# Kernel optimization log

Hardware: AMD Instinct MI355X
Metric: run time of the kernel (lower is better)

Reference implementation:

```python
import jax, jax.numpy as jnp
import numpy as np

B = 2
H = 112
W = 112
C = 256
NHEAD = 8
SW = 7          # strip width
WIN = 2 * SW    # 14, window size of attn3
L = H * W
HID = 4 * C     # mlp hidden


def _rel_pos_index(wh, ww):
    coords = np.stack(np.meshgrid(np.arange(wh), np.arange(ww), indexing='ij'))  # (2, wh, ww)
    cf = coords.reshape(2, -1)
    rel = (cf[:, :, None] - cf[:, None, :]).transpose(1, 2, 0)  # (N, N, 2)
    rel[:, :, 0] += wh - 1
    rel[:, :, 1] += ww - 1
    rel[:, :, 0] *= 2 * ww - 1
    return rel.sum(-1)  # (N, N) int


def setup_inputs() -> dict:
    key = jax.random.key(0)
    ks = jax.random.split(key, 16)
    s = 0.02
    d = {}
    d['x'] = jax.random.normal(ks[0], (B, L, C), jnp.float32)
    d['g1'] = jnp.ones((C,), jnp.float32); d['b1'] = jnp.zeros((C,), jnp.float32)
    d['g2'] = jnp.ones((C,), jnp.float32); d['b2'] = jnp.zeros((C,), jnp.float32)
    for i, p in enumerate(['a1', 'a2', 'a3']):
        d[p + '_wqkv'] = jax.random.normal(ks[1 + i], (C, 3 * C), jnp.float32) * s
        d[p + '_wproj'] = jax.random.normal(ks[4 + i], (C, C), jnp.float32) * s
        d[p + '_bproj'] = jnp.zeros((C,), jnp.float32)
    d['a3_rpb'] = jax.random.normal(ks[7], ((2 * WIN - 1) * (2 * WIN - 1), NHEAD), jnp.float32) * s
    d['w_fc1'] = jax.random.normal(ks[8], (C, HID), jnp.float32) * s
    d['b_fc1'] = jnp.zeros((HID,), jnp.float32)
    d['w_fc2'] = jax.random.normal(ks[9], (HID, C), jnp.float32) * s
    d['b_fc2'] = jnp.zeros((C,), jnp.float32)
    return d


def _ln(x, g, b):
    m = x.mean(-1, keepdims=True)
    v = jnp.mean((x - m) ** 2, axis=-1, keepdims=True)
    return (x - m) * jax.lax.rsqrt(v + 1e-5) * g + b


def _mha(xw, wqkv, wproj, bproj, bias=None):
    # xw: (Bw, N, C) -> vanilla MHA within each window
    Bw, N, Cc = xw.shape
    hd = Cc // NHEAD
    qkv = (xw @ wqkv).reshape(Bw, N, 3, NHEAD, hd).transpose(2, 0, 3, 1, 4)
    q, k, v = qkv[0], qkv[1], qkv[2]
    attn = jnp.einsum('bhnd,bhmd->bhnm', q, k) * (hd ** -0.5)
    if bias is not None:
        attn = attn + bias
    attn = jax.nn.softmax(attn, axis=-1)
    out = jnp.einsum('bhnm,bhmd->bhnd', attn, v).transpose(0, 2, 1, 3).reshape(Bw, N, Cc)
    return out @ wproj + bproj


def _forward(x, g1, b1, g2, b2,
             a1_wqkv, a1_wproj, a1_bproj,
             a2_wqkv, a2_wproj, a2_bproj,
             a3_wqkv, a3_wproj, a3_bproj, a3_rpb,
             w_fc1, b_fc1, w_fc2, b_fc2):
    shortcut = x
    xn = _ln(x, g1, b1)
    xg = xn.reshape(B, H, W, C)

    # attn1: horizontal strips, window (SW, W) -> seq SW*W
    xh = xg.reshape(B * (H // SW), SW * W, C)
    x1 = _mha(xh, a1_wqkv, a1_wproj, a1_bproj).reshape(B, L, C)

    # attn2: vertical strips, window (H, SW) -> seq H*SW
    xv = xg.reshape(B, H, W // SW, SW, C).transpose(0, 2, 1, 3, 4).reshape(B * (W // SW), H * SW, C)
    x2 = _mha(xv, a2_wqkv, a2_wproj, a2_bproj)
    x2 = x2.reshape(B, W // SW, H, SW, C).transpose(0, 2, 1, 3, 4).reshape(B, L, C)

    # attn3: 14x14 windows with relative position bias
    xw = xg.reshape(B, H // WIN, WIN, W // WIN, WIN, C).transpose(0, 1, 3, 2, 4, 5).reshape(-1, WIN * WIN, C)
    rpi = jnp.asarray(_rel_pos_index(WIN, WIN).reshape(-1))
    bias = a3_rpb[rpi].reshape(WIN * WIN, WIN * WIN, NHEAD).transpose(2, 0, 1)[None]  # (1,h,N,N)
    x3 = _mha(xw, a3_wqkv, a3_wproj, a3_bproj, bias=bias)
    x3 = x3.reshape(B, H // WIN, W // WIN, WIN, WIN, C).transpose(0, 1, 3, 2, 4, 5).reshape(B, L, C)

    # attention-based aggregation of the three branches (per token)
    kx = jnp.stack([x1, x2, x3], axis=2)                      # (B, L, 3, C)
    scores = jnp.einsum('blc,blkc->blk', xn, kx) * (C ** -0.5)
    wts = jax.nn.softmax(scores, axis=-1)
    f = jnp.einsum('blk,blkc->blc', wts, kx)

    x = shortcut + f
    h = jax.nn.gelu(_ln(x, g2, b2) @ w_fc1 + b_fc1, approximate=False) @ w_fc2 + b_fc2
    return x + h


def reference(x, g1, b1, g2, b2,
              a1_wqkv, a1_wproj, a1_bproj,
              a2_wqkv, a2_wproj, a2_bproj,
              a3_wqkv, a3_wproj, a3_bproj, a3_rpb,
              w_fc1, b_fc1, w_fc2, b_fc2):
    return _forward(x, g1, b1, g2, b2,
                    a1_wqkv, a1_wproj, a1_bproj,
                    a2_wqkv, a2_wproj, a2_bproj,
                    a3_wqkv, a3_wproj, a3_bproj, a3_rpb,
                    w_fc1, b_fc1, w_fc2, b_fc2)
```

## Files before the change

kernel.cpp:

```cpp
#include <hip/hip_runtime.h>
#include <hip/hip_bf16.h>

#define M_TOK   25088
#define C_DIM   256
#define NH      8
#define HID_DIM 1024
#define PSTR    40
#define ASTR    40
#define LOG2E   1.4426950408889634f
#define MC_ELT  ((size_t)M_TOK * C_DIM)

typedef __attribute__((ext_vector_type(8))) short short8;
typedef __attribute__((ext_vector_type(4))) short short4v;
typedef __attribute__((ext_vector_type(4))) float f32x4;
typedef __attribute__((ext_vector_type(4))) unsigned u32x4;

__device__ __forceinline__ short f2bf(float f) {
    return __builtin_bit_cast(short, __float2bfloat16(f));
}
__device__ __forceinline__ float bf2f(short s) {
    return __bfloat162float(__builtin_bit_cast(__hip_bfloat16, s));
}

__device__ __forceinline__ int xcd_swz(int orig, int nwg) {
    int q = nwg >> 3, r = nwg & 7;
    int xcd = orig & 7, sub = orig >> 3;
    return (xcd < r ? xcd * (q + 1) : r * (q + 1) + (xcd - r) * q) + sub;
}

__device__ __forceinline__ int map_t(int branch, int w, int n) {
    if (branch == 0) {
        return w * 784 + n;
    } else if (branch == 1) {
        int b = w >> 4, wc = w & 15;
        int h2 = n / 7, s = n - h2 * 7;
        return b * 12544 + h2 * 112 + wc * 7 + s;
    } else {
        int b = w >> 6, wi = w & 63;
        int wh = wi >> 3, ww = wi & 7;
        int i = n / 14, j = n - i * 14;
        return b * 12544 + (wh * 14 + i) * 112 + ww * 14 + j;
    }
}

__device__ __forceinline__ int win2tok(int br, int m) {
    if (br == 0) return m;
    if (br == 1) { int w = m / 784, n = m - w * 784; return map_t(1, w, n); }
    int w = m / 196, n = m - w * 196; return map_t(2, w, n);
}

template<int BR>
__device__ __forceinline__ void tok2win(int t, int& w, int& n) {
    if constexpr (BR == 0) {
        w = t / 784; n = t - w * 784;
    } else if constexpr (BR == 1) {
        int b = t / 12544, r = t - b * 12544;
        int h2 = r / 112, cc = r - h2 * 112;
        int wc = cc / 7, s = cc - wc * 7;
        w = b * 16 + wc; n = h2 * 7 + s;
    } else {
        int b = t / 12544, r = t - b * 12544;
        int ii = r / 112, jj = r - ii * 112;
        int wh = ii / 14, i = ii - wh * 14;
        int ww = jj / 14, j = jj - ww * 14;
        w = b * 64 + wh * 8 + ww; n = i * 14 + j;
    }
}
__device__ __forceinline__ void tok2win_rt(int br, int t, int& w, int& n) {
    if (br == 0) tok2win<0>(t, w, n);
    else if (br == 1) tok2win<1>(t, w, n);
    else tok2win<2>(t, w, n);
}

__global__ void detect_kernel(const unsigned* __restrict__ g1, int* flag) {
    if (threadIdx.x == 0) *flag = (g1[0] == 0x3F800000u) ? 1 : 0;
}

struct PrepArgs {
    const void* src[9];
    short* dst[9];
    int n[9];
};
__global__ void prep_kernel(PrepArgs a, const int* __restrict__ flag) {
    int i = blockIdx.x * 256 + threadIdx.x;
    int fp32 = *flag;
    #pragma unroll
    for (int s = 0; s < 9; ++s) {
        if (i < a.n[s]) {
            a.dst[s][i] = fp32 ? f2bf(((const float*)a.src[s])[i])
                               : ((const short*)a.src[s])[i];
            return;
        }
        i -= a.n[s];
    }
}

__global__ void biasmat_kernel(const void* __restrict__ rpbr,
                               short* __restrict__ bmat,
                               const int* __restrict__ flag) {
    int idx = blockIdx.x * 256 + threadIdx.x;
    if (idx >= 8 * 196 * 196) return;
    int h = idx / 38416, rest = idx - h * 38416;
    int n1 = rest / 196, n2 = rest - n1 * 196;
    int i1 = n1 / 14, j1 = n1 - i1 * 14;
    int i2 = n2 / 14, j2 = n2 - i2 * 14;
    int src = ((i1 - i2 + 13) * 27 + (j1 - j2 + 13)) * 8 + h;
    float v = *flag ? ((const float*)rpbr)[src] : bf2f(((const short*)rpbr)[src]);
    bmat[idx] = f2bf(v * LOG2E);
}

__global__ __launch_bounds__(256) void ln_kernel(
    const void* __restrict__ x, const short* __restrict__ g,
    const short* __restrict__ b, short* __restrict__ out,
    const int* __restrict__ flag)
{
    int t = blockIdx.x * 4 + (threadIdx.x >> 6);
    int lane = threadIdx.x & 63;
    size_t base = (size_t)t * C_DIM + lane * 4;
    float v[4];
    if (*flag) {
        f32x4 hv = *(const f32x4*)((const float*)x + base);
        #pragma unroll
        for (int j = 0; j < 4; ++j) v[j] = hv[j];
    } else {
        short4v hv = *(const short4v*)((const short*)x + base);
        #pragma unroll
        for (int j = 0; j < 4; ++j) v[j] = bf2f(hv[j]);
    }
    float s = v[0] + v[1] + v[2] + v[3];
    float ss = v[0]*v[0] + v[1]*v[1] + v[2]*v[2] + v[3]*v[3];
    for (int off = 32; off; off >>= 1) {
        s  += __shfl_xor(s, off);
        ss += __shfl_xor(ss, off);
    }
    float mean = s * (1.f / 256.f);
    float var  = fmaxf(ss * (1.f / 256.f) - mean * mean, 0.f);
    float rstd = rsqrtf(var + 1e-5f);
    short4v hg = *(const short4v*)(g + lane * 4);
    short4v hb = *(const short4v*)(b + lane * 4);
    short4v o;
    #pragma unroll
    for (int j = 0; j < 4; ++j)
        o[j] = f2bf((v[j] - mean) * rstd * bf2f(hg[j]) + bf2f(hb[j]));
    *(short4v*)(out + base) = o;
}

struct TJobs {
    const void* src[8];
    short* dst[8];
    int R[8], C[8], sc[8], tx[8];
    int pre[9];
    float smul;
};
__global__ void transpose_all_kernel(TJobs jb, const int* __restrict__ flag)
{
    __shared__ short tile[32][33];
    int b = blockIdx.x;
    int j = 0;
    while (b >= jb.pre[j + 1]) ++j;
    int local = b - jb.pre[j];
    int tX = jb.tx[j];
    int c0 = (local % tX) * 32, r0 = (local / tX) * 32;
    const void* src = jb.src[j];
    short* dst = jb.dst[j];
    int R = jb.R[j], Cc = jb.C[j], scaleCols = jb.sc[j];
    int tx_ = threadIdx.x, ty_ = threadIdx.y;
    int fp32 = *flag;
    #pragma unroll
    for (int i = 0; i < 32; i += 8) {
        int r = r0 + ty_ + i, c = c0 + tx_;
        if (r < R && c < Cc) {
            size_t idx = (size_t)r * Cc + c;
            float v = fp32 ? ((const float*)src)[idx] : bf2f(((const short*)src)[idx]);
            if (c < scaleCols) v *= jb.smul;
            tile[ty_ + i][tx_] = f2bf(v);
        }
    }
    __syncthreads();
    #pragma unroll
    for (int i = 0; i < 32; i += 8) {
        int r = c0 + ty_ + i, c = r0 + tx_;
        if (r < Cc && c < R) dst[(size_t)r * R + c] = tile[tx_][ty_ + i];
    }
}

__device__ __forceinline__ float fast_gelu(float v) {
    float v2 = v * v;
    float a = v * (2.30221856f + 0.102948668f * v2);
    float e2 = __builtin_amdgcn_exp2f(-a);
    return v * __builtin_amdgcn_rcpf(1.f + e2);
}

template<int QKV>
__global__ __launch_bounds__(512, 4) void gemm256_kernel(
    const short* __restrict__ A, const short* __restrict__ Bt,
    short* __restrict__ Out, int Nn, int Kk,
    const short* __restrict__ bias, int act, short* __restrict__ qkvb)
{
    __shared__ alignas(16) short As[2][256 * ASTR];
    __shared__ alignas(16) short Bs[2][128 * ASTR];
    int tid = threadIdx.x;
    int lane = tid & 63, wid = tid >> 6;
    int wrow = (wid >> 1) * 64, wcol = (wid & 1) * 64;
    int r16 = lane & 15, q4 = lane >> 4;

    int gX = gridDim.x;
    int nwg = gX * gridDim.y;
    int wgid = xcd_swz(blockIdx.y * gX + blockIdx.x, nwg);
    int bx = wgid % gX, by = wgid / gX;
    int mb = by * 256, nb = bx * 128;

    int arow = tid >> 1, ash = (tid & 1) * 16;
    int brow = tid >> 2, bsh = (tid & 3) * 8;
    const short* Ag = A  + (size_t)(mb + arow) * Kk + ash;
    const short* Bg = Bt + (size_t)(nb + brow) * Kk + bsh;
    short* Al = &As[0][arow * ASTR + ash];
    short* Bl = &Bs[0][brow * ASTR + bsh];

    f32x4 acc[4][4];
    #pragma unroll
    for (int i = 0; i < 4; ++i)
        #pragma unroll
        for (int j = 0; j < 4; ++j)
            acc[i][j] = (f32x4){0.f, 0.f, 0.f, 0.f};

    {
        short8 a0 = *(const short8*)(Ag);
        short8 a1 = *(const short8*)(Ag + 8);
        short8 b0 = *(const short8*)(Bg);
        *(short8*)(Al)     = a0;
        *(short8*)(Al + 8) = a1;
        *(short8*)(Bl)     = b0;
    }
    __syncthreads();

    int nk = Kk >> 5;
    for (int ki = 0; ki < nk; ++ki) {
        int cur = ki & 1;
        bool pref = (ki + 1 < nk);
        short8 na0, na1, nb0;
        if (pref) {
            int k0 = (ki + 1) << 5;
            na0 = *(const short8*)(Ag + k0);
            na1 = *(const short8*)(Ag + k0 + 8);
            nb0 = *(const short8*)(Bg + k0);
        }
        const short* Ar = &As[cur][0];
        const short* Br = &Bs[cur][0];
        short8 af[4], bf[4];
        #pragma unroll
        for (int mi = 0; mi < 4; ++mi)
            af[mi] = *(const short8*)(Ar + (wrow + mi * 16 + r16) * ASTR + q4 * 8);
        #pragma unroll
        for (int ni = 0; ni < 4; ++ni)
            bf[ni] = *(const short8*)(Br + (wcol + ni * 16 + r16) * ASTR + q4 * 8);
        __builtin_amdgcn_s_setprio(1);
        #pragma unroll
        for (int mi = 0; mi < 4; ++mi)
            #pragma unroll
            for (int ni = 0; ni < 4; ++ni)
                acc[mi][ni] = __builtin_amdgcn_mfma_f32_16x16x32_bf16(af[mi], bf[ni], acc[mi][ni], 0, 0, 0);
        __builtin_amdgcn_s_setprio(0);
        if (pref) {
            *(short8*)(Al + (cur ^ 1) * (256 * ASTR))     = na0;
            *(short8*)(Al + (cur ^ 1) * (256 * ASTR) + 8) = na1;
            *(short8*)(Bl + (cur ^ 1) * (128 * ASTR))     = nb0;
        }
        __syncthreads();
    }

    if constexpr (QKV == 0) {
        #pragma unroll
        for (int mi = 0; mi < 4; ++mi) {
            #pragma unroll
            for (int ni = 0; ni < 4; ++ni) {
                int n = nb + wcol + ni * 16 + r16;
                float bval = bias ? bf2f(bias[n]) : 0.f;
                #pragma unroll
                for (int r = 0; r < 4; ++r) {
                    int m = mb + wrow + mi * 16 + q4 * 4 + r;
                    float v = acc[mi][ni][r] + bval;
                    if (act == 1) v = fast_gelu(v);
                    Out[(size_t)m * Nn + n] = f2bf(v);
                }
            }
        }
    } else {
        int brq = nb / 768;
        int rem = nb - brq * 768;
        int sel = rem >> 8;
        int colb = rem & 255;
        int Nw = (brq == 2) ? 196 : 784;
        short* dst = qkvb + ((size_t)brq * 3 + sel) * MC_ELT + colb;
        #pragma unroll
        for (int mi = 0; mi < 4; ++mi) {
            #pragma unroll
            for (int r = 0; r < 4; ++r) {
                int m = mb + wrow + mi * 16 + q4 * 4 + r;
                int w, nwin;
                tok2win_rt(brq, m, w, nwin);
                size_t row = (size_t)(w * Nw + nwin) * 256;
                #pragma unroll
                for (int ni = 0; ni < 4; ++ni)
                    dst[row + wcol + ni * 16 + r16] = f2bf(acc[mi][ni][r]);
            }
        }
    }
}

__global__ __launch_bounds__(256) void gemm128_kernel(
    const short* __restrict__ A, const short* __restrict__ Bt,
    void* __restrict__ Out, int Nn, int Kk,
    const short* __restrict__ bias, const short* __restrict__ res,
    const int* __restrict__ oflag)
{
    __shared__ alignas(16) short As[2][128 * ASTR];
    __shared__ alignas(16) short Bs[2][128 * ASTR];
    int tid = threadIdx.x;
    int lane = tid & 63, wid = tid >> 6;
    int wrow = (wid >> 1) * 64, wcol = (wid & 1) * 64;
    int r16 = lane & 15, q4 = lane >> 4;

    int gX = gridDim.x;
    int nwg = gX * gridDim.y;
    int wgid = xcd_swz(blockIdx.y * gX + blockIdx.x, nwg);
    int bx = wgid % gX, by = wgid / gX;
    int mb = by * 128, nb = bx * 128;

    int srow = tid >> 1, sh = (tid & 1) * 16;
    const short* Ag = A  + (size_t)(mb + srow) * Kk + sh;
    const short* Bg = Bt + (size_t)(nb + srow) * Kk + sh;
    short* Al = &As[0][srow * ASTR + sh];
    short* Bl = &Bs[0][srow * ASTR + sh];

    f32x4 acc[4][4];
    #pragma unroll
    for (int i = 0; i < 4; ++i)
        #pragma unroll
        for (int j = 0; j < 4; ++j)
            acc[i][j] = (f32x4){0.f, 0.f, 0.f, 0.f};

    {
        short8 a0 = *(const short8*)(Ag);
        short8 a1 = *(const short8*)(Ag + 8);
        short8 b0 = *(const short8*)(Bg);
        short8 b1 = *(const short8*)(Bg + 8);
        *(short8*)(Al)     = a0;
        *(short8*)(Al + 8) = a1;
        *(short8*)(Bl)     = b0;
        *(short8*)(Bl + 8) = b1;
    }
    __syncthreads();

    int nk = Kk >> 5;
    for (int ki = 0; ki < nk; ++ki) {
        int cur = ki & 1;
        bool pref = (ki + 1 < nk);
        short8 na0, na1, nb0, nb1;
        if (pref) {
            int k0 = (ki + 1) << 5;
            na0 = *(const short8*)(Ag + k0);
            na1 = *(const short8*)(Ag + k0 + 8);
            nb0 = *(const short8*)(Bg + k0);
            nb1 = *(const short8*)(Bg + k0 + 8);
        }
        const short* Ar = &As[cur][0];
        const short* Br = &Bs[cur][0];
        short8 af[4], bf[4];
        #pragma unroll
        for (int mi = 0; mi < 4; ++mi)
            af[mi] = *(const short8*)(Ar + (wrow + mi * 16 + r16) * ASTR + q4 * 8);
        #pragma unroll
        for (int ni = 0; ni < 4; ++ni)
            bf[ni] = *(const short8*)(Br + (wcol + ni * 16 + r16) * ASTR + q4 * 8);
        __builtin_amdgcn_s_setprio(1);
        #pragma unroll
        for (int mi = 0; mi < 4; ++mi)
            #pragma unroll
            for (int ni = 0; ni < 4; ++ni)
                acc[mi][ni] = __builtin_amdgcn_mfma_f32_16x16x32_bf16(af[mi], bf[ni], acc[mi][ni], 0, 0, 0);
        __builtin_amdgcn_s_setprio(0);
        if (pref) {
            int off2 = (cur ^ 1) * (128 * ASTR);
            *(short8*)(Al + off2)     = na0;
            *(short8*)(Al + off2 + 8) = na1;
            *(short8*)(Bl + off2)     = nb0;
            *(short8*)(Bl + off2 + 8) = nb1;
        }
        __syncthreads();
    }

    int ofp32 = oflag ? *oflag : 0;
    #pragma unroll
    for (int mi = 0; mi < 4; ++mi) {
        #pragma unroll
        for (int ni = 0; ni < 4; ++ni) {
            int n = nb + wcol + ni * 16 + r16;
            float bval = bias ? bf2f(bias[n]) : 0.f;
            #pragma unroll
            for (int r = 0; r < 4; ++r) {
                int m = mb + wrow + mi * 16 + q4 * 4 + r;
                float v = acc[mi][ni][r] + bval;
                if (res) v += bf2f(res[(size_t)m * Nn + n]);
                size_t oi = (size_t)m * Nn + n;
                if (ofp32) ((float*)Out)[oi] = v;
                else       ((short*)Out)[oi] = f2bf(v);
            }
        }
    }
}

__global__ __launch_bounds__(256) void gemm_proj_kernel(
    const short* __restrict__ awb, const short* __restrict__ wprojT,
    const short* __restrict__ bproj3, short* __restrict__ pbb)
{
    __shared__ alignas(16) short As[2][128 * ASTR];
    __shared__ alignas(16) short Bs[2][128 * ASTR];
    int tid = threadIdx.x;
    int lane = tid & 63, wid = tid >> 6;
    int wrow = (wid >> 1) * 64, wcol = (wid & 1) * 64;
    int r16 = lane & 15, q4 = lane >> 4;
    int br = blockIdx.z;

    const short* A  = awb + (size_t)br * MC_ELT;
    const short* Bt = wprojT + (size_t)br * 256 * 256;
    const short* bias = bproj3 + br * 256;
    short* Out = pbb + (size_t)br * MC_ELT;

    int gX = gridDim.x;
    int nwg = gX * gridDim.y;
    int wgid = xcd_swz(blockIdx.y * gX + blockIdx.x, nwg);
    int bx = wgid % gX, by = wgid / gX;
    int mb = by * 128, nb = bx * 128;

    int srow = tid >> 1, sh = (tid & 1) * 16;
    const short* Ag = A  + (size_t)(mb + srow) * 256 + sh;
    const short* Bg = Bt + (size_t)(nb + srow) * 256 + sh;
    short* Al = &As[0][srow * ASTR + sh];
    short* Bl = &Bs[0][srow * ASTR + sh];

    f32x4 acc[4][4];
    #pragma unroll
    for (int i = 0; i < 4; ++i)
        #pragma unroll
        for (int j = 0; j < 4; ++j)
            acc[i][j] = (f32x4){0.f, 0.f, 0.f, 0.f};

    {
        short8 a0 = *(const short8*)(Ag);
        short8 a1 = *(const short8*)(Ag + 8);
        short8 b0 = *(const short8*)(Bg);
        short8 b1 = *(const short8*)(Bg + 8);
        *(short8*)(Al)     = a0;
        *(short8*)(Al + 8) = a1;
        *(short8*)(Bl)     = b0;
        *(short8*)(Bl + 8) = b1;
    }
    __syncthreads();

    #pragma unroll
    for (int ki = 0; ki < 8; ++ki) {
        int cur = ki & 1;
        bool pref = (ki + 1 < 8);
        short8 na0, na1, nb0, nb1;
        if (pref) {
            int k0 = (ki + 1) << 5;
            na0 = *(const short8*)(Ag + k0);
            na1 = *(const short8*)(Ag + k0 + 8);
            nb0 = *(const short8*)(Bg + k0);
            nb1 = *(const short8*)(Bg + k0 + 8);
        }
        const short* Ar = &As[cur][0];
        const short* Br = &Bs[cur][0];
        short8 af[4], bf[4];
        #pragma unroll
        for (int mi = 0; mi < 4; ++mi)
            af[mi] = *(const short8*)(Ar + (wrow + mi * 16 + r16) * ASTR + q4 * 8);
        #pragma unroll
        for (int ni = 0; ni < 4; ++ni)
            bf[ni] = *(const short8*)(Br + (wcol + ni * 16 + r16) * ASTR + q4 * 8);
        __builtin_amdgcn_s_setprio(1);
        #pragma unroll
        for (int mi = 0; mi < 4; ++mi)
            #pragma unroll
            for (int ni = 0; ni < 4; ++ni)
                acc[mi][ni] = __builtin_amdgcn_mfma_f32_16x16x32_bf16(af[mi], bf[ni], acc[mi][ni], 0, 0, 0);
        __builtin_amdgcn_s_setprio(0);
        if (pref) {
            int off2 = (cur ^ 1) * (128 * ASTR);
            *(short8*)(Al + off2)     = na0;
            *(short8*)(Al + off2 + 8) = na1;
            *(short8*)(Bl + off2)     = nb0;
            *(short8*)(Bl + off2 + 8) = nb1;
        }
        __syncthreads();
    }

    #pragma unroll
    for (int mi = 0; mi < 4; ++mi) {
        #pragma unroll
        for (int r = 0; r < 4; ++r) {
            int m = mb + wrow + mi * 16 + q4 * 4 + r;
            int t = win2tok(br, m);
            size_t row = (size_t)t * 256;
            #pragma unroll
            for (int ni = 0; ni < 4; ++ni) {
                int n = nb + wcol + ni * 16 + r16;
                Out[row + n] = f2bf(acc[mi][ni][r] + bf2f(bias[n]));
            }
        }
    }
}

__global__ __launch_bounds__(256) void attn_kernel(
    const short* __restrict__ qkvb, const short* __restrict__ bmat,
    short* __restrict__ awb)
{
    __shared__ alignas(16) short kbuf[2][64 * PSTR];
    __shared__ alignas(16) short vbuf[2][2048];

    int tid = threadIdx.x;
    int lane = tid & 63, wid = tid >> 6;
    int bid = xcd_swz(blockIdx.x, gridDim.x);
    int br, N, QC;
    const short* bmp = nullptr;
    if (bid < 1792)      { br = 0; N = 784; QC = 7; }
    else if (bid < 3584) { br = 1; N = 784; QC = 7; bid -= 1792; }
    else                 { br = 2; N = 196; QC = 2; bid -= 3584; bmp = bmat; }
    const short* qw = qkvb + (size_t)br * 3 * MC_ELT;
    const short* kw = qw + MC_ELT;
    const short* vw = qw + 2 * MC_ELT;
    short* aw = awb + (size_t)br * MC_ELT;

    int t2 = bid / QC;
    int qc = bid - t2 * QC;
    int h = t2 & 7;
    int w = t2 >> 3;
    int qt = qc * 4 + wid;
    int r16 = lane & 15, q4 = lane >> 4;
    int wbase = w * N;
    int QT = (N + 31) >> 5;
    bool active = (qt < QT);

    const short* kws = kw + (size_t)wbase * 256 + h * 32;
    const short* vws = vw + (size_t)wbase * 256 + h * 32;

    int s_row = tid >> 2, s_seg = tid & 3;
    int s_k = s_row & 31;
    int Lr = (s_row >> 5) * 32 + ((s_k & 15) >> 2) * 8 + (s_k >> 4) * 4 + (s_k & 3);
    short* kdst = &kbuf[0][s_row * PSTR + s_seg * 8];
    short* vdst = &vbuf[0][(s_seg >> 1) * 1024 + Lr * 16 + (s_seg & 1) * 8];
    const short* ksrc = kws + s_seg * 8;
    const short* vsrc = vws + s_seg * 8;

    int qr0 = qt * 32 + r16;      if (qr0 >= N) qr0 = N - 1;
    int qr1 = qt * 32 + 16 + r16; if (qr1 >= N) qr1 = N - 1;
    short8 aq0 = *(const short8*)(qw + (size_t)(wbase + qr0) * 256 + h * 32 + q4 * 8);
    short8 aq1 = *(const short8*)(qw + (size_t)(wbase + qr1) * 256 + h * 32 + q4 * 8);

    f32x4 o00 = {0.f,0.f,0.f,0.f}, o01 = o00, o10 = o00, o11 = o00;
    float psA = 0.f, psB = 0.f;
    const short* bra = nullptr; const short* brb = nullptr;
    if (bmp) {
        const short* bh = bmp + (size_t)h * 38416;
        int n1a = qt * 32 + r16;      if (n1a >= N) n1a = N - 1;
        int n1b = qt * 32 + 16 + r16; if (n1b >= N) n1b = N - 1;
        bra = bh + n1a * 196;
        brb = bh + n1b * 196;
    }
    f32x4 zero = {0.f,0.f,0.f,0.f};
    unsigned vb0 = (unsigned)(unsigned long long)(&vbuf[0][0]) + q4 * 256 + r16 * 2;

    int nch = (N + 63) >> 6;
    {
        *(short8*)kdst = *(const short8*)(ksrc + (size_t)s_row * 256);
        *(short8*)vdst = *(const short8*)(vsrc + (size_t)s_row * 256);
    }
    __syncthreads();

    for (int cb = 0; cb < nch; ++cb) {
        int cur = cb & 1;
        bool pref = (cb + 1 < nch);
        short8 kreg, vreg;
        if (pref) {
            int r = (cb + 1) * 64 + s_row; if (r >= N) r = N - 1;
            kreg = *(const short8*)(ksrc + (size_t)r * 256);
            vreg = *(const short8*)(vsrc + (size_t)r * 256);
        }
        if (active) {
            int kb0 = cb * 64;
            int kb1 = kb0 + 32;
            bool act1 = (kb1 < N);
            const short* kbc = &kbuf[cur][0];
            short8 bk00 = *(const short8*)(kbc + r16 * PSTR + q4 * 8);
            short8 bk01 = *(const short8*)(kbc + (16 + r16) * PSTR + q4 * 8);
            short8 bk10 = *(const short8*)(kbc + (32 + r16) * PSTR + q4 * 8);
            short8 bk11 = *(const short8*)(kbc + (48 + r16) * PSTR + q4 * 8);
            unsigned va = vb0 + cur * 4096;
            short4v t00, t01, t02, t03, t10, t11, t12, t13;
            asm volatile("ds_read_b64_tr_b16 %0, %1"             : "=v"(t00) : "v"(va));
            asm volatile("ds_read_b64_tr_b16 %0, %1 offset:128"  : "=v"(t01) : "v"(va));
            asm volatile("ds_read_b64_tr_b16 %0, %1 offset:2048" : "=v"(t02) : "v"(va));
            asm volatile("ds_read_b64_tr_b16 %0, %1 offset:2176" : "=v"(t03) : "v"(va));
            asm volatile("ds_read_b64_tr_b16 %0, %1 offset:1024" : "=v"(t10) : "v"(va));
            asm volatile("ds_read_b64_tr_b16 %0, %1 offset:1152" : "=v"(t11) : "v"(va));
            asm volatile("ds_read_b64_tr_b16 %0, %1 offset:3072" : "=v"(t12) : "v"(va));
            asm volatile("ds_read_b64_tr_b16 %0, %1 offset:3200" : "=v"(t13) : "v"(va));
            short4v hb00, hb01, hb02, hb03, hb10, hb11, hb12, hb13;
            if (bmp) {
                int k00 = kb0 + q4 * 4, k01 = k00 + 16;
                int k10 = kb1 + q4 * 4, k11 = k10 + 16;
                k00 = (k00 <= N - 4) ? k00 : N - 4;
                k01 = (k01 <= N - 4) ? k01 : N - 4;
                k10 = (k10 <= N - 4) ? k10 : N - 4;
                k11 = (k11 <= N - 4) ? k11 : N - 4;
                hb00 = *(const short4v*)(bra + k00);
                hb01 = *(const short4v*)(bra + k01);
                hb02 = *(const short4v*)(brb + k00);
                hb03 = *(const short4v*)(brb + k01);
                hb10 = *(const short4v*)(bra + k10);
                hb11 = *(const short4v*)(bra + k11);
                hb12 = *(const short4v*)(brb + k10);
                hb13 = *(const short4v*)(brb + k11);
            }
            asm volatile("s_waitcnt lgkmcnt(0)" ::: "memory");
            __builtin_amdgcn_sched_barrier(0);

            f32x4 sa0, sb0, sc0, sd0, sa1, sb1, sc1, sd1;
            __builtin_amdgcn_s_setprio(1);
            sa0 = __builtin_amdgcn_mfma_f32_16x16x32_bf16(bk00, aq0, zero, 0, 0, 0);
            sb0 = __builtin_amdgcn_mfma_f32_16x16x32_bf16(bk01, aq0, zero, 0, 0, 0);
            sc0 = __builtin_amdgcn_mfma_f32_16x16x32_bf16(bk00, aq1, zero, 0, 0, 0);
            sd0 = __builtin_amdgcn_mfma_f32_16x16x32_bf16(bk01, aq1, zero, 0, 0, 0);
            if (act1) {
                sa1 = __builtin_amdgcn_mfma_f32_16x16x32_bf16(bk10, aq0, zero, 0, 0, 0);
                sb1 = __builtin_amdgcn_mfma_f32_16x16x32_bf16(bk11, aq0, zero, 0, 0, 0);
                sc1 = __builtin_amdgcn_mfma_f32_16x16x32_bf16(bk10, aq1, zero, 0, 0, 0);
                sd1 = __builtin_amdgcn_mfma_f32_16x16x32_bf16(bk11, aq1, zero, 0, 0, 0);
            }
            __builtin_amdgcn_s_setprio(0);

            int k0 = kb0 + q4 * 4, k1 = k0 + 16;
            if (bmp) {
                #pragma unroll
                for (int r = 0; r < 4; ++r) {
                    sa0[r] += bf2f(hb00[r]); sb0[r] += bf2f(hb01[r]);
                    sc0[r] += bf2f(hb02[r]); sd0[r] += bf2f(hb03[r]);
                }
            }
            if (kb0 + 32 > N) {
                #pragma unroll
                for (int r = 0; r < 4; ++r) {
                    if (k0 + r >= N) { sa0[r] = -30000.f; sc0[r] = -30000.f; }
                    if (k1 + r >= N) { sb0[r] = -30000.f; sd0[r] = -30000.f; }
                }
            }
            float ea[4], eb[4], ec[4], ed[4];
            #pragma unroll
            for (int r = 0; r < 4; ++r) {
                ea[r] = __builtin_amdgcn_exp2f(sa0[r]);
                eb[r] = __builtin_amdgcn_exp2f(sb0[r]);
                ec[r] = __builtin_amdgcn_exp2f(sc0[r]);
                ed[r] = __builtin_amdgcn_exp2f(sd0[r]);
                psA += ea[r] + eb[r];
                psB += ec[r] + ed[r];
            }
            unsigned w00, w01, w02, w03, w10, w11, w12, w13;
            asm("v_cvt_pk_bf16_f32 %0, %1, %2" : "=v"(w00) : "v"(ea[0]), "v"(ea[1]));
            asm("v_cvt_pk_bf16_f32 %0, %1, %2" : "=v"(w01) : "v"(ea[2]), "v"(ea[3]));
            asm("v_cvt_pk_bf16_f32 %0, %1, %2" : "=v"(w02) : "v"(eb[0]), "v"(eb[1]));
            asm("v_cvt_pk_bf16_f32 %0, %1, %2" : "=v"(w03) : "v"(eb[2]), "v"(eb[3]));
            asm("v_cvt_pk_bf16_f32 %0, %1, %2" : "=v"(w10) : "v"(ec[0]), "v"(ec[1]));
            asm("v_cvt_pk_bf16_f32 %0, %1, %2" : "=v"(w11) : "v"(ec[2]), "v"(ec[3]));
            asm("v_cvt_pk_bf16_f32 %0, %1, %2" : "=v"(w12) : "v"(ed[0]), "v"(ed[1]));
            asm("v_cvt_pk_bf16_f32 %0, %1, %2" : "=v"(w13) : "v"(ed[2]), "v"(ed[3]));
            u32x4 u0 = {w00, w01, w02, w03};
            u32x4 u1 = {w10, w11, w12, w13};
            short8 pa0 = __builtin_bit_cast(short8, u0);
            short8 pa1 = __builtin_bit_cast(short8, u1);
            short8 bv0, bv1;
            #pragma unroll
            for (int j = 0; j < 4; ++j) {
                bv0[j] = t00[j]; bv0[4 + j] = t01[j];
                bv1[j] = t02[j]; bv1[4 + j] = t03[j];
            }
            __builtin_amdgcn_s_setprio(1);
            o00 = __builtin_amdgcn_mfma_f32_16x16x32_bf16(pa0, bv0, o00, 0, 0, 0);
            o01 = __builtin_amdgcn_mfma_f32_16x16x32_bf16(pa0, bv1, o01, 0, 0, 0);
            o10 = __builtin_amdgcn_mfma_f32_16x16x32_bf16(pa1, bv0, o10, 0, 0, 0);
            o11 = __builtin_amdgcn_mfma_f32_16x16x32_bf16(pa1, bv1, o11, 0, 0, 0);
            __builtin_amdgcn_s_setprio(0);

            if (act1) {
                int k2 = kb1 + q4 * 4, k3 = k2 + 16;
                if (bmp) {
                    #pragma unroll
                    for (int r = 0; r < 4; ++r) {
                        sa1[r] += bf2f(hb10[r]); sb1[r] += bf2f(hb11[r]);
                        sc1[r] += bf2f(hb12[r]); sd1[r] += bf2f(hb13[r]);
                    }
                }
                if (kb1 + 32 > N) {
                    #pragma unroll
                    for (int r = 0; r < 4; ++r) {
                        if (k2 + r >= N) { sa1[r] = -30000.f; sc1[r] = -30000.f; }
                        if (k3 + r >= N) { sb1[r] = -30000.f; sd1[r] = -30000.f; }
                    }
                }
                #pragma unroll
                for (int r = 0; r < 4; ++r) {
                    ea[r] = __builtin_amdgcn_exp2f(sa1[r]);
                    eb[r] = __builtin_amdgcn_exp2f(sb1[r]);
                    ec[r] = __builtin_amdgcn_exp2f(sc1[r]);
                    ed[r] = __builtin_amdgcn_exp2f(sd1[r]);
                    psA += ea[r] + eb[r];
                    psB += ec[r] + ed[r];
                }
                asm("v_cvt_pk_bf16_f32 %0, %1, %2" : "=v"(w00) : "v"(ea[0]), "v"(ea[1]));
                asm("v_cvt_pk_bf16_f32 %0, %1, %2" : "=v"(w01) : "v"(ea[2]), "v"(ea[3]));
                asm("v_cvt_pk_bf16_f32 %0, %1, %2" : "=v"(w02) : "v"(eb[0]), "v"(eb[1]));
                asm("v_cvt_pk_bf16_f32 %0, %1, %2" : "=v"(w03) : "v"(eb[2]), "v"(eb[3]));
                asm("v_cvt_pk_bf16_f32 %0, %1, %2" : "=v"(w10) : "v"(ec[0]), "v"(ec[1]));
                asm("v_cvt_pk_bf16_f32 %0, %1, %2" : "=v"(w11) : "v"(ec[2]), "v"(ec[3]));
                asm("v_cvt_pk_bf16_f32 %0, %1, %2" : "=v"(w12) : "v"(ed[0]), "v"(ed[1]));
                asm("v_cvt_pk_bf16_f32 %0, %1, %2" : "=v"(w13) : "v"(ed[2]), "v"(ed[3]));
                u32x4 u2 = {w00, w01, w02, w03};
                u32x4 u3 = {w10, w11, w12, w13};
                short8 pb0 = __builtin_bit_cast(short8, u2);
                short8 pb1 = __builtin_bit_cast(short8, u3);
                short8 cv0, cv1;
                #pragma unroll
                for (int j = 0; j < 4; ++j) {
                    cv0[j] = t10[j]; cv0[4 + j] = t11[j];
                    cv1[j] = t12[j]; cv1[4 + j] = t13[j];
                }
                __builtin_amdgcn_s_setprio(1);
                o00 = __builtin_amdgcn_mfma_f32_16x16x32_bf16(pb0, cv0, o00, 0, 0, 0);
                o01 = __builtin_amdgcn_mfma_f32_16x16x32_bf16(pb0, cv1, o01, 0, 0, 0);
                o10 = __builtin_amdgcn_mfma_f32_16x16x32_bf16(pb1, cv0, o10, 0, 0, 0);
                o11 = __builtin_amdgcn_mfma_f32_16x16x32_bf16(pb1, cv1, o11, 0, 0, 0);
                __builtin_amdgcn_s_setprio(0);
            }
        }
        if (pref) {
            *(short8*)(kdst + ((cb + 1) & 1) * (64 * PSTR)) = kreg;
            *(short8*)(vdst + ((cb + 1) & 1) * 2048) = vreg;
        }
        __syncthreads();
    }

    if (active) {
        psA += __shfl_xor(psA, 16); psA += __shfl_xor(psA, 32);
        psB += __shfl_xor(psB, 16); psB += __shfl_xor(psB, 32);
        float invA = 1.f / fmaxf(psA, 1e-20f);
        float invB = 1.f / fmaxf(psB, 1e-20f);
        #pragma unroll
        for (int r = 0; r < 4; ++r) {
            float i0 = __shfl(invA, q4 * 4 + r);
            float i1 = __shfl(invB, q4 * 4 + r);
            int n1 = qt * 32 + q4 * 4 + r;
            if (n1 < N) {
                size_t row = (size_t)(wbase + n1) * 256;
                aw[row + h * 32 + r16]      = f2bf(o00[r] * i0);
                aw[row + h * 32 + 16 + r16] = f2bf(o01[r] * i0);
            }
            int n2 = n1 + 16;
            if (n2 < N) {
                size_t row = (size_t)(wbase + n2) * 256;
                aw[row + h * 32 + r16]      = f2bf(o10[r] * i1);
                aw[row + h * 32 + 16 + r16] = f2bf(o11[r] * i1);
            }
        }
    }
}

__global__ __launch_bounds__(256) void agg_kernel(
    const void* __restrict__ x, const short* __restrict__ xn,
    const short* __restrict__ pbb, short* __restrict__ yout,
    short* __restrict__ xn2, const short* __restrict__ g2,
    const short* __restrict__ b2, const int* __restrict__ flag)
{
    int t = blockIdx.x * 4 + (threadIdx.x >> 6);
    int lane = threadIdx.x & 63;
    size_t base = (size_t)t * C_DIM + lane * 4;
    short4v hn = *(const short4v*)(xn + base);
    short4v h0 = *(const short4v*)(pbb + base);
    short4v h1 = *(const short4v*)(pbb + MC_ELT + base);
    short4v h2 = *(const short4v*)(pbb + 2 * MC_ELT + base);
    float nv[4], v0[4], v1[4], v2[4];
    #pragma unroll
    for (int j = 0; j < 4; ++j) {
        nv[j] = bf2f(hn[j]); v0[j] = bf2f(h0[j]);
        v1[j] = bf2f(h1[j]); v2[j] = bf2f(h2[j]);
    }
    float d0 = 0.f, d1 = 0.f, d2 = 0.f;
    #pragma unroll
    for (int j = 0; j < 4; ++j) {
        d0 += nv[j] * v0[j]; d1 += nv[j] * v1[j]; d2 += nv[j] * v2[j];
    }
    for (int off = 32; off; off >>= 1) {
        d0 += __shfl_xor(d0, off);
        d1 += __shfl_xor(d1, off);
        d2 += __shfl_xor(d2, off);
    }
    d0 *= 0.0625f; d1 *= 0.0625f; d2 *= 0.0625f;
    float m = fmaxf(fmaxf(d0, d1), d2);
    float e0 = __expf(d0 - m), e1 = __expf(d1 - m), e2 = __expf(d2 - m);
    float inv = 1.f / (e0 + e1 + e2);
    e0 *= inv; e1 *= inv; e2 *= inv;

    float vx[4];
    if (*flag) {
        f32x4 hv = *(const f32x4*)((const float*)x + base);
        #pragma unroll
        for (int j = 0; j < 4; ++j) vx[j] = hv[j];
    } else {
        short4v hv = *(const short4v*)((const short*)x + base);
        #pragma unroll
        for (int j = 0; j < 4; ++j) vx[j] = bf2f(hv[j]);
    }
    float vy[4];
    #pragma unroll
    for (int j = 0; j < 4; ++j)
        vy[j] = vx[j] + e0 * v0[j] + e1 * v1[j] + e2 * v2[j];
    float s = 0.f, ss = 0.f;
    #pragma unroll
    for (int j = 0; j < 4; ++j) { s += vy[j]; ss += vy[j] * vy[j]; }
    for (int off = 32; off; off >>= 1) {
        s  += __shfl_xor(s, off);
        ss += __shfl_xor(ss, off);
    }
    float mean = s * (1.f / 256.f);
    float var  = fmaxf(ss * (1.f / 256.f) - mean * mean, 0.f);
    float rstd = rsqrtf(var + 1e-5f);
    short4v hg = *(const short4v*)(g2 + lane * 4);
    short4v hb = *(const short4v*)(b2 + lane * 4);
    short4v oy, on;
    #pragma unroll
    for (int j = 0; j < 4; ++j) {
        oy[j] = f2bf(vy[j]);
        on[j] = f2bf((vy[j] - mean) * rstd * bf2f(hg[j]) + bf2f(hb[j]));
    }
    *(short4v*)(yout + base) = oy;
    *(short4v*)(xn2  + base) = on;
}

extern "C" void kernel_launch(void* const* d_in, const int* in_sizes, int n_in,
                              void* d_out, int out_size, void* d_ws, size_t ws_size,
                              hipStream_t stream)
{
    const void* x   = d_in[0];
    const void* g1r = d_in[1];
    const void* b1r = d_in[2];
    const void* g2r = d_in[3];
    const void* b2r = d_in[4];
    const void* wqkv[3]   = {d_in[5], d_in[8],  d_in[11]};
    const void* wproj[3]  = {d_in[6], d_in[9],  d_in[12]};
    const void* bprojr[3] = {d_in[7], d_in[10], d_in[13]};
    const void* rpbr  = d_in[14];
    const void* wfc1  = d_in[15];
    const void* bfc1r = d_in[16];
    const void* wfc2  = d_in[17];
    const void* bfc2r = d_in[18];

    char* ws = (char*)d_ws;
    size_t off = 0;
    auto give = [&](size_t bytes) -> char* {
        char* p = ws + off;
        off += (bytes + 255) & ~(size_t)255;
        return p;
    };
    int*   flag = (int*)give(256);
    short* xn   = (short*)give(MC_ELT * 2);
    short* yb   = (short*)give(MC_ELT * 2);
    short* g1 = (short*)give(256 * 2), *b1 = (short*)give(256 * 2);
    short* g2 = (short*)give(256 * 2), *b2 = (short*)give(256 * 2);
    short* bproj3 = (short*)give(3 * 256 * 2);
    short* bfc1 = (short*)give(1024 * 2), *bfc2 = (short*)give(256 * 2);
    short* bmat = (short*)give((size_t)8 * 196 * 196 * 2);
    short* wqkvT  = (short*)give((size_t)3 * 768 * 256 * 2);
    short* wprojT = (short*)give((size_t)3 * 256 * 256 * 2);
    short* fc1T = (short*)give(1024 * 256 * 2);
    short* fc2T = (short*)give(256 * 1024 * 2);
    short* qkvb = (short*)give((size_t)9 * MC_ELT * 2);
    short* awb  = (short*)give((size_t)3 * MC_ELT * 2);
    short* pbb  = (short*)give((size_t)3 * MC_ELT * 2);
    short* hbuf = qkvb;

    const float scale = 0.17677669529663687f * LOG2E;

    detect_kernel<<<1, 64, 0, stream>>>((const unsigned*)g1r, flag);
    PrepArgs pa;
    pa.src[0] = g1r;  pa.dst[0] = g1;  pa.n[0] = 256;
    pa.src[1] = b1r;  pa.dst[1] = b1;  pa.n[1] = 256;
    pa.src[2] = g2r;  pa.dst[2] = g2;  pa.n[2] = 256;
    pa.src[3] = b2r;  pa.dst[3] = b2;  pa.n[3] = 256;
    pa.src[4] = bprojr[0]; pa.dst[4] = bproj3;       pa.n[4] = 256;
    pa.src[5] = bprojr[1]; pa.dst[5] = bproj3 + 256; pa.n[5] = 256;
    pa.src[6] = bprojr[2]; pa.dst[6] = bproj3 + 512; pa.n[6] = 256;
    pa.src[7] = bfc1r; pa.dst[7] = bfc1; pa.n[7] = 1024;
    pa.src[8] = bfc2r; pa.dst[8] = bfc2; pa.n[8] = 256;
    prep_kernel<<<12, 256, 0, stream>>>(pa, flag);
    biasmat_kernel<<<(8 * 196 * 196 + 255) / 256, 256, 0, stream>>>(rpbr, bmat, flag);

    TJobs tj;
    tj.smul = scale;
    int pre = 0;
    for (int i = 0; i < 3; ++i) {
        tj.src[i] = wqkv[i]; tj.dst[i] = wqkvT + (size_t)i * 768 * 256;
        tj.R[i] = 256; tj.C[i] = 768; tj.sc[i] = 256; tj.tx[i] = 24;
        tj.pre[i] = pre; pre += 24 * 8;
    }
    for (int i = 0; i < 3; ++i) {
        tj.src[3 + i] = wproj[i]; tj.dst[3 + i] = wprojT + (size_t)i * 256 * 256;
        tj.R[3 + i] = 256; tj.C[3 + i] = 256; tj.sc[3 + i] = 0; tj.tx[3 + i] = 8;
        tj.pre[3 + i] = pre; pre += 8 * 8;
    }
    tj.src[6] = wfc1; tj.dst[6] = fc1T;
    tj.R[6] = 256; tj.C[6] = 1024; tj.sc[6] = 0; tj.tx[6] = 32;
    tj.pre[6] = pre; pre += 32 * 8;
    tj.src[7] = wfc2; tj.dst[7] = fc2T;
    tj.R[7] = 1024; tj.C[7] = 256; tj.sc[7] = 0; tj.tx[7] = 8;
    tj.pre[7] = pre; pre += 8 * 32;
    tj.pre[8] = pre;
    transpose_all_kernel<<<pre, dim3(32, 8), 0, stream>>>(tj, flag);

    ln_kernel<<<M_TOK / 4, 256, 0, stream>>>(x, g1, b1, xn, flag);

    gemm256_kernel<1><<<dim3(18, M_TOK / 256), 512, 0, stream>>>(
        xn, wqkvT, nullptr, 2304, 256, nullptr, 0, qkvb);

    attn_kernel<<<5632, 256, 0, stream>>>(qkvb, bmat, awb);

    gemm_proj_kernel<<<dim3(2, M_TOK / 128, 3), 256, 0, stream>>>(
        awb, wprojT, bproj3, pbb);

    agg_kernel<<<M_TOK / 4, 256, 0, stream>>>(
        x, xn, pbb, yb, xn, g2, b2, flag);

    gemm256_kernel<0><<<dim3(8, M_TOK / 256), 512, 0, stream>>>(
        xn, fc1T, hbuf, 1024, 256, bfc1, 1, nullptr);
    gemm128_kernel<<<dim3(2, M_TOK / 128), 256, 0, stream>>>(
        hbuf, fc2T, d_out, 256, 1024, bfc2, yb, flag);
}
```

Before: 392.1 us.

## Use 8-wave attention blocks and compute softmax row sums with MFMA

Each attention block grows from 4 to 8 waves, so one block covers more query tiles of a (window, head) pair and shares a single K/V staging pass. Each staging thread now loads either K or V rather than both. The softmax denominator is accumulated by extra MFMAs against a ones vector, which replaces the per-lane adds, cross-lane shuffles and division with a direct reciprocal. The trade-offs are wasted inactive waves in the 196-token branch (7 tiles on 8 waves), more MFMA work per chunk, and row sums taken from bf16-rounded probabilities.

```diff
diff --git a/kernel.cpp b/kernel.cpp
--- a/kernel.cpp
+++ b/kernel.cpp
@@ -512,7 +512,7 @@
     }
 }
 
-__global__ __launch_bounds__(256) void attn_kernel(
+__global__ __launch_bounds__(512) void attn_kernel(
     const short* __restrict__ qkvb, const short* __restrict__ bmat,
     short* __restrict__ awb)
 {
@@ -524,9 +524,9 @@
     int bid = xcd_swz(blockIdx.x, gridDim.x);
     int br, N, QC;
     const short* bmp = nullptr;
-    if (bid < 1792)      { br = 0; N = 784; QC = 7; }
-    else if (bid < 3584) { br = 1; N = 784; QC = 7; bid -= 1792; }
-    else                 { br = 2; N = 196; QC = 2; bid -= 3584; bmp = bmat; }
+    if (bid < 1024)      { br = 0; N = 784; QC = 4; }
+    else if (bid < 2048) { br = 1; N = 784; QC = 4; bid -= 1024; }
+    else                 { br = 2; N = 196; QC = 1; bid -= 2048; bmp = bmat; }
     const short* qw = qkvb + (size_t)br * 3 * MC_ELT;
     const short* kw = qw + MC_ELT;
     const short* vw = qw + 2 * MC_ELT;
@@ -536,7 +536,7 @@
     int qc = bid - t2 * QC;
     int h = t2 & 7;
     int w = t2 >> 3;
-    int qt = qc * 4 + wid;
+    int qt = qc * 8 + wid;
     int r16 = lane & 15, q4 = lane >> 4;
     int wbase = w * N;
     int QT = (N + 31) >> 5;
@@ -545,13 +545,15 @@
     const short* kws = kw + (size_t)wbase * 256 + h * 32;
     const short* vws = vw + (size_t)wbase * 256 + h * 32;
 
-    int s_row = tid >> 2, s_seg = tid & 3;
+    int slot = tid & 255;
+    int s_row = slot >> 2, s_seg = slot & 3;
     int s_k = s_row & 31;
     int Lr = (s_row >> 5) * 32 + ((s_k & 15) >> 2) * 8 + (s_k >> 4) * 4 + (s_k & 3);
-    short* kdst = &kbuf[0][s_row * PSTR + s_seg * 8];
-    short* vdst = &vbuf[0][(s_seg >> 1) * 1024 + Lr * 16 + (s_seg & 1) * 8];
-    const short* ksrc = kws + s_seg * 8;
-    const short* vsrc = vws + s_seg * 8;
+    bool isV = tid >= 256;
+    short* s_dst = isV ? &vbuf[0][(s_seg >> 1) * 1024 + Lr * 16 + (s_seg & 1) * 8]
+                       : &kbuf[0][s_row * PSTR + s_seg * 8];
+    int s_bstride = isV ? 2048 : 64 * PSTR;
+    const short* s_src = (isV ? vws : kws) + s_seg * 8;
 
     int qr0 = qt * 32 + r16;      if (qr0 >= N) qr0 = N - 1;
     int qr1 = qt * 32 + 16 + r16; if (qr1 >= N) qr1 = N - 1;
@@ -559,7 +561,11 @@
     short8 aq1 = *(const short8*)(qw + (size_t)(wbase + qr1) * 256 + h * 32 + q4 * 8);
 
     f32x4 o00 = {0.f,0.f,0.f,0.f}, o01 = o00, o10 = o00, o11 = o00;
-    float psA = 0.f, psB = 0.f;
+    f32x4 osum0 = o00, osum1 = o00;
+    short8 ones;
+    #pragma unroll
+    for (int j = 0; j < 8; ++j) ones[j] = (short)0x3F80;
+
     const short* bra = nullptr; const short* brb = nullptr;
     if (bmp) {
         const short* bh = bmp + (size_t)h * 38416;
@@ -573,19 +579,17 @@
 
     int nch = (N + 63) >> 6;
     {
-        *(short8*)kdst = *(const short8*)(ksrc + (size_t)s_row * 256);
-        *(short8*)vdst = *(const short8*)(vsrc + (size_t)s_row * 256);
+        *(short8*)s_dst = *(const short8*)(s_src + (size_t)s_row * 256);
     }
     __syncthreads();
 
     for (int cb = 0; cb < nch; ++cb) {
         int cur = cb & 1;
         bool pref = (cb + 1 < nch);
-        short8 kreg, vreg;
+        short8 sreg;
         if (pref) {
             int r = (cb + 1) * 64 + s_row; if (r >= N) r = N - 1;
-            kreg = *(const short8*)(ksrc + (size_t)r * 256);
-            vreg = *(const short8*)(vsrc + (size_t)r * 256);
+            sreg = *(const short8*)(s_src + (size_t)r * 256);
         }
         if (active) {
             int kb0 = cb * 64;
@@ -662,8 +666,6 @@
                 eb[r] = __builtin_amdgcn_exp2f(sb0[r]);
                 ec[r] = __builtin_amdgcn_exp2f(sc0[r]);
                 ed[r] = __builtin_amdgcn_exp2f(sd0[r]);
-                psA += ea[r] + eb[r];
-                psB += ec[r] + ed[r];
             }
             unsigned w00, w01, w02, w03, w10, w11, w12, w13;
             asm("v_cvt_pk_bf16_f32 %0, %1, %2" : "=v"(w00) : "v"(ea[0]), "v"(ea[1]));
@@ -689,6 +691,8 @@
             o01 = __builtin_amdgcn_mfma_f32_16x16x32_bf16(pa0, bv1, o01, 0, 0, 0);
             o10 = __builtin_amdgcn_mfma_f32_16x16x32_bf16(pa1, bv0, o10, 0, 0, 0);
             o11 = __builtin_amdgcn_mfma_f32_16x16x32_bf16(pa1, bv1, o11, 0, 0, 0);
+            osum0 = __builtin_amdgcn_mfma_f32_16x16x32_bf16(pa0, ones, osum0, 0, 0, 0);
+            osum1 = __builtin_amdgcn_mfma_f32_16x16x32_bf16(pa1, ones, osum1, 0, 0, 0);
             __builtin_amdgcn_s_setprio(0);
 
             if (act1) {
@@ -713,8 +717,6 @@
                     eb[r] = __builtin_amdgcn_exp2f(sb1[r]);
                     ec[r] = __builtin_amdgcn_exp2f(sc1[r]);
                     ed[r] = __builtin_amdgcn_exp2f(sd1[r]);
-                    psA += ea[r] + eb[r];
-                    psB += ec[r] + ed[r];
                 }
                 asm("v_cvt_pk_bf16_f32 %0, %1, %2" : "=v"(w00) : "v"(ea[0]), "v"(ea[1]));
                 asm("v_cvt_pk_bf16_f32 %0, %1, %2" : "=v"(w01) : "v"(ea[2]), "v"(ea[3]));
@@ -739,25 +741,21 @@
                 o01 = __builtin_amdgcn_mfma_f32_16x16x32_bf16(pb0, cv1, o01, 0, 0, 0);
                 o10 = __builtin_amdgcn_mfma_f32_16x16x32_bf16(pb1, cv0, o10, 0, 0, 0);
                 o11 = __builtin_amdgcn_mfma_f32_16x16x32_bf16(pb1, cv1, o11, 0, 0, 0);
+                osum0 = __builtin_amdgcn_mfma_f32_16x16x32_bf16(pb0, ones, osum0, 0, 0, 0);
+                osum1 = __builtin_amdgcn_mfma_f32_16x16x32_bf16(pb1, ones, osum1, 0, 0, 0);
                 __builtin_amdgcn_s_setprio(0);
             }
         }
-        if (pref) {
-            *(short8*)(kdst + ((cb + 1) & 1) * (64 * PSTR)) = kreg;
-            *(short8*)(vdst + ((cb + 1) & 1) * 2048) = vreg;
-        }
+        if (pref)
+            *(short8*)(s_dst + ((cb + 1) & 1) * s_bstride) = sreg;
         __syncthreads();
     }
 
     if (active) {
-        psA += __shfl_xor(psA, 16); psA += __shfl_xor(psA, 32);
-        psB += __shfl_xor(psB, 16); psB += __shfl_xor(psB, 32);
-        float invA = 1.f / fmaxf(psA, 1e-20f);
-        float invB = 1.f / fmaxf(psB, 1e-20f);
         #pragma unroll
         for (int r = 0; r < 4; ++r) {
-            float i0 = __shfl(invA, q4 * 4 + r);
-            float i1 = __shfl(invB, q4 * 4 + r);
+            float i0 = __builtin_amdgcn_rcpf(fmaxf(osum0[r], 1e-20f));
+            float i1 = __builtin_amdgcn_rcpf(fmaxf(osum1[r], 1e-20f));
             int n1 = qt * 32 + q4 * 4 + r;
             if (n1 < N) {
                 size_t row = (size_t)(wbase + n1) * 256;
@@ -930,7 +928,7 @@
     gemm256_kernel<1><<<dim3(18, M_TOK / 256), 512, 0, stream>>>(
         xn, wqkvT, nullptr, 2304, 256, nullptr, 0, qkvb);
 
-    attn_kernel<<<5632, 256, 0, stream>>>(qkvb, bmat, awb);
+    attn_kernel<<<3072, 512, 0, stream>>>(qkvb, bmat, awb);
 
     gemm_proj_kernel<<<dim3(2, M_TOK / 128, 3), 256, 0, stream>>>(
         awb, wprojT, bproj3, pbb);
```

New measurement: 425.2 us. +8.5%, slower.
